# Kernel tuning notes

Measured on AMD Instinct MI355X. Metric: run time of the kernel, lower is better.

Reference implementation:

```python
import jax, jax.numpy as jnp
import numpy as np

D, HEADS, LVLS, PTS, DFF = 256, 8, 4, 4, 1024
LQ, B = 900, 16
SHAPES = [(100, 100), (50, 50), (25, 25), (13, 13)]
S = sum(h * w for h, w in SHAPES)  # 13294
EPS = 1e-5


def layer_norm(x, g, b):
    m = jnp.mean(x, -1, keepdims=True)
    v = jnp.mean((x - m) ** 2, -1, keepdims=True)
    return (x - m) * jax.lax.rsqrt(v + EPS) * g + b


def bilinear_gather(value_l, loc, H_, W_):
    # value_l: (b,h,H_,W_,dh); loc: (b,h,Lq,P,2) normalized to [0,1]
    b, h, _, _, dh = value_l.shape
    Lq, P = loc.shape[2], loc.shape[3]
    # grid_sample align_corners=False, padding_mode='zeros' semantics
    x = loc[..., 0] * W_ - 0.5
    y = loc[..., 1] * H_ - 0.5
    x0 = jnp.floor(x); y0 = jnp.floor(y)
    wx = x - x0; wy = y - y0
    x0i = x0.astype(jnp.int32); y0i = y0.astype(jnp.int32)
    vflat = value_l.reshape(b, h, H_ * W_, dh)

    def corner(xi, yi, w):
        valid = (xi >= 0) & (xi < W_) & (yi >= 0) & (yi < H_)
        idx = jnp.clip(yi, 0, H_ - 1) * W_ + jnp.clip(xi, 0, W_ - 1)
        g = jnp.take_along_axis(vflat, idx.reshape(b, h, Lq * P)[..., None], axis=2)
        return g.reshape(b, h, Lq, P, dh) * (w * valid)[..., None]

    return (corner(x0i, y0i, (1 - wx) * (1 - wy)) + corner(x0i + 1, y0i, wx * (1 - wy))
            + corner(x0i, y0i + 1, (1 - wx) * wy) + corner(x0i + 1, y0i + 1, wx * wy))


def setup_inputs() -> dict:
    key = jax.random.key(0)
    ks = jax.random.split(key, 32)
    w = lambda k, *s: (jax.random.normal(k, s, jnp.float32) * 0.02)
    shapes = jnp.array(SHAPES, jnp.int32)
    starts = jnp.array(np.cumsum([0] + [h_ * w_ for h_, w_ in SHAPES[:-1]]), jnp.int32)
    return {
        'tgt': jax.random.normal(ks[0], (LQ, B, D), jnp.float32),
        'tgt_query_pos': jax.random.normal(ks[1], (LQ, B, D), jnp.float32),
        'tgt_reference_points': jax.random.uniform(ks[2], (LQ, B, LVLS, 4), jnp.float32, 0.05, 0.95),
        'memory': jax.random.normal(ks[3], (S, B, D), jnp.float32),
        'memory_spatial_shapes': shapes,
        'memory_level_start_index': starts,
        # self-attn (nn.MultiheadAttention)
        'in_proj_w': w(ks[4], 3 * D, D), 'in_proj_b': jnp.zeros((3 * D,), jnp.float32),
        'sa_out_w': w(ks[5], D, D), 'sa_out_b': jnp.zeros((D,), jnp.float32),
        # MSDeformAttn
        'off_w': w(ks[6], HEADS * LVLS * PTS * 2, D), 'off_b': w(ks[7], HEADS * LVLS * PTS * 2),
        'aw_w': w(ks[8], HEADS * LVLS * PTS, D), 'aw_b': jnp.zeros((HEADS * LVLS * PTS,), jnp.float32),
        'val_w': w(ks[9], D, D), 'val_b': jnp.zeros((D,), jnp.float32),
        'ca_out_w': w(ks[10], D, D), 'ca_out_b': jnp.zeros((D,), jnp.float32),
        # FFN
        'lin1_w': w(ks[11], DFF, D), 'lin1_b': jnp.zeros((DFF,), jnp.float32),
        'lin2_w': w(ks[12], D, DFF), 'lin2_b': jnp.zeros((D,), jnp.float32),
        # norms (norm2 after sa, norm1 after ca, norm3 after ffn)
        'norm1_g': jnp.ones((D,), jnp.float32), 'norm1_b': jnp.zeros((D,), jnp.float32),
        'norm2_g': jnp.ones((D,), jnp.float32), 'norm2_b': jnp.zeros((D,), jnp.float32),
        'norm3_g': jnp.ones((D,), jnp.float32), 'norm3_b': jnp.zeros((D,), jnp.float32),
    }


def reference(tgt, tgt_query_pos, tgt_reference_points, memory,
              memory_spatial_shapes, memory_level_start_index,
              in_proj_w, in_proj_b, sa_out_w, sa_out_b,
              off_w, off_b, aw_w, aw_b, val_w, val_b, ca_out_w, ca_out_b,
              lin1_w, lin1_b, lin2_w, lin2_b,
              norm1_g, norm1_b, norm2_g, norm2_b, norm3_g, norm3_b):
    Lq, b, d = tgt.shape
    h = HEADS
    dh = d // h
    shapes = np.asarray(memory_spatial_shapes)  # static level shapes
    starts = np.asarray(memory_level_start_index)

    # ---- self-attention (module_seq[0] = 'sa') ----
    qk = tgt + tgt_query_pos  # pos on q,k only
    Wq, Wk, Wv = jnp.split(in_proj_w, 3, axis=0)
    bq, bk, bv = jnp.split(in_proj_b, 3)
    to_heads = lambda x: x.transpose(1, 0, 2).reshape(b, Lq, h, dh).transpose(0, 2, 1, 3)
    qh = to_heads(qk @ Wq.T + bq)
    kh = to_heads(qk @ Wk.T + bk)
    vh = to_heads(tgt @ Wv.T + bv)
    attn = jax.nn.softmax(jnp.einsum('bhqd,bhkd->bhqk', qh, kh) / jnp.sqrt(jnp.float32(dh)), axis=-1)
    sa = jnp.einsum('bhqk,bhkd->bhqd', attn, vh).transpose(0, 2, 1, 3).reshape(b, Lq, d).transpose(1, 0, 2)
    sa = sa @ sa_out_w.T + sa_out_b
    tgt = layer_norm(tgt + sa, norm2_g, norm2_b)

    # ---- deformable cross-attention (MSDeformAttn) ----
    query = (tgt + tgt_query_pos).transpose(1, 0, 2)            # (b,Lq,d)
    ref = tgt_reference_points.transpose(1, 0, 2, 3)            # (b,Lq,L,4)
    value = (memory.transpose(1, 0, 2) @ val_w.T + val_b).reshape(b, -1, h, dh)  # (b,S,h,dh)
    off = (query @ off_w.T + off_b).reshape(b, Lq, h, LVLS, PTS, 2)
    aw = jax.nn.softmax((query @ aw_w.T + aw_b).reshape(b, Lq, h, LVLS * PTS), axis=-1)
    aw = aw.reshape(b, Lq, h, LVLS, PTS).transpose(0, 2, 1, 3, 4)  # (b,h,Lq,L,P)
    # 4-dim refs: loc = xy + off/P * wh * 0.5
    loc = ref[:, :, None, :, None, :2] + off / PTS * ref[:, :, None, :, None, 2:] * 0.5
    loc = loc.transpose(0, 2, 1, 3, 4, 5)                        # (b,h,Lq,L,P,2)

    out = jnp.zeros((b, h, Lq, dh), jnp.float32)
    for l in range(LVLS):
        H_, W_ = int(shapes[l, 0]), int(shapes[l, 1])
        s0 = int(starts[l])
        value_l = value[:, s0:s0 + H_ * W_].reshape(b, H_, W_, h, dh).transpose(0, 3, 1, 2, 4)
        samp = bilinear_gather(value_l, loc[:, :, :, l], H_, W_)   # (b,h,Lq,P,dh)
        out = out + jnp.einsum('bhqpd,bhqp->bhqd', samp, aw[:, :, :, l])
    ca = out.transpose(0, 2, 1, 3).reshape(b, Lq, d) @ ca_out_w.T + ca_out_b
    ca = ca.transpose(1, 0, 2)
    tgt = layer_norm(tgt + ca, norm1_g, norm1_b)

    # ---- FFN (intended math: linear2(relu(linear1(tgt)))) ----
    t2 = jnp.maximum(tgt @ lin1_w.T + lin1_b, 0.0) @ lin2_w.T + lin2_b
    tgt = layer_norm(tgt + t2, norm3_g, norm3_b)
    return tgt
```

## Files before the change

kernel.cpp:

```cpp
#include <hip/hip_runtime.h>
#include <hip/hip_bf16.h>
#include <math.h>

#define D_ 256
#define HEADS_ 8
#define DH_ 32
#define LVLS_ 4
#define PTS_ 4
#define DFF_ 1024
#define LQ_ 900
#define B_ 16
#define S_ 13294
#define MQ (LQ_*B_)
#define MV (S_*B_)

typedef __attribute__((ext_vector_type(4))) float f32x4;
typedef __attribute__((ext_vector_type(8))) short bf16x8;

static __device__ inline ushort f2bf(float f) {
  __hip_bfloat16 h = __float2bfloat16(f);
  union { __hip_bfloat16 h; ushort u; } c; c.h = h;
  return c.u;
}
static __device__ inline float bf2f(ushort u) {
  union { float f; uint u; } c; c.u = (uint)u << 16; return c.f;
}

#define GP 40

__global__ __launch_bounds__(512) void gemm_bf16_512(
    const float* __restrict__ A, const float* __restrict__ Wm,
    const float* __restrict__ bias, float* __restrict__ Y,
    int M, int N, int K, int relu, int outbf)
{
  __shared__ ushort As[128 * GP];
  __shared__ ushort Ws[128 * GP];
  const int tid  = threadIdx.x;
  const int lane = tid & 63;
  const int wid  = tid >> 6;
  const int wr   = wid >> 1;
  const int wc   = wid & 1;
  const int fr = lane & 15;
  const int fk = (lane >> 4) << 3;
  const int m0 = blockIdx.y * 128, n0 = blockIdx.x * 128;

  f32x4 acc[2][4];
  const f32x4 zero = {0.f, 0.f, 0.f, 0.f};
#pragma unroll
  for (int i = 0; i < 2; ++i)
#pragma unroll
    for (int j = 0; j < 4; ++j) acc[i][j] = zero;

  const int srow = tid >> 2;
  const int skh  = (tid & 3) << 3;
  int agr = m0 + srow; if (agr > M - 1) agr = M - 1;
  const float* apb = A  + (size_t)agr * K + skh;
  const float* wpb = Wm + (size_t)(n0 + srow) * K + skh;

  float4 pa[2], pw[2];
  pa[0] = *(const float4*)(apb);     pa[1] = *(const float4*)(apb + 4);
  pw[0] = *(const float4*)(wpb);     pw[1] = *(const float4*)(wpb + 4);

  for (int k0 = 0; k0 < K; k0 += 32) {
    if (k0) __syncthreads();
    ushort tmp[8] __attribute__((aligned(16)));
    tmp[0]=f2bf(pa[0].x); tmp[1]=f2bf(pa[0].y); tmp[2]=f2bf(pa[0].z); tmp[3]=f2bf(pa[0].w);
    tmp[4]=f2bf(pa[1].x); tmp[5]=f2bf(pa[1].y); tmp[6]=f2bf(pa[1].z); tmp[7]=f2bf(pa[1].w);
    *(bf16x8*)&As[srow*GP + skh] = *(const bf16x8*)tmp;
    tmp[0]=f2bf(pw[0].x); tmp[1]=f2bf(pw[0].y); tmp[2]=f2bf(pw[0].z); tmp[3]=f2bf(pw[0].w);
    tmp[4]=f2bf(pw[1].x); tmp[5]=f2bf(pw[1].y); tmp[6]=f2bf(pw[1].z); tmp[7]=f2bf(pw[1].w);
    *(bf16x8*)&Ws[srow*GP + skh] = *(const bf16x8*)tmp;
    if (k0 + 32 < K) {
      const float* ap = apb + k0 + 32;
      const float* wp = wpb + k0 + 32;
      pa[0] = *(const float4*)(ap);  pa[1] = *(const float4*)(ap + 4);
      pw[0] = *(const float4*)(wp);  pw[1] = *(const float4*)(wp + 4);
    }
    __syncthreads();

    bf16x8 ar[2], br[4];
#pragma unroll
    for (int i = 0; i < 2; ++i)
      ar[i] = *(const bf16x8*)&As[(wr*32 + i*16 + fr)*GP + fk];
#pragma unroll
    for (int j = 0; j < 4; ++j)
      br[j] = *(const bf16x8*)&Ws[(wc*64 + j*16 + fr)*GP + fk];
#pragma unroll
    for (int i = 0; i < 2; ++i)
#pragma unroll
      for (int j = 0; j < 4; ++j)
        acc[i][j] = __builtin_amdgcn_mfma_f32_16x16x32_bf16(ar[i], br[j], acc[i][j], 0, 0, 0);
  }

  const int gcolbase = n0 + wc * 64 + fr;
  float bias4[4];
#pragma unroll
  for (int j = 0; j < 4; ++j) bias4[j] = bias[gcolbase + j * 16];
#pragma unroll
  for (int i = 0; i < 2; ++i) {
    const int rb = m0 + wr * 32 + i * 16 + (lane >> 4) * 4;
#pragma unroll
    for (int r = 0; r < 4; ++r) {
      const int grow = rb + r;
      if (grow < M) {
#pragma unroll
        for (int j = 0; j < 4; ++j) {
          float v = acc[i][j][r] + bias4[j];
          if (relu) v = fmaxf(v, 0.f);
          if (outbf) ((ushort*)Y)[(size_t)grow * N + gcolbase + j * 16] = f2bf(v);
          else       Y[(size_t)grow * N + gcolbase + j * 16] = v;
        }
      }
    }
  }
}

__global__ __launch_bounds__(256) void gemm_bf16_64(
    const float* __restrict__ A, const float* __restrict__ X2,
    const float* __restrict__ Wm, const float* __restrict__ bias,
    float* __restrict__ Y, int M, int N, int K, int relu, int outbf)
{
  __shared__ ushort As[64 * GP];
  __shared__ ushort Ws[64 * GP];
  const int tid  = threadIdx.x;
  const int lane = tid & 63;
  const int wid  = tid >> 6;
  const int wr = wid >> 1, wc = wid & 1;
  const int fr = lane & 15;
  const int fk = (lane >> 4) << 3;
  const int m0 = blockIdx.y * 64, n0 = blockIdx.x * 64;

  f32x4 acc[2][2];
  const f32x4 zero = {0.f, 0.f, 0.f, 0.f};
#pragma unroll
  for (int i = 0; i < 2; ++i)
#pragma unroll
    for (int j = 0; j < 2; ++j) acc[i][j] = zero;

  const int srow = tid >> 1;
  const int skh  = (tid & 1) << 4;
  const bool isA = srow < 64;
  const float* src;
  const float* src2 = nullptr;
  ushort* dst;
  if (isA) {
    int gr = m0 + srow; if (gr > M - 1) gr = M - 1;
    src = A + (size_t)gr * K + skh;
    if (X2) src2 = X2 + (size_t)gr * K + skh;
    dst = &As[srow * GP + skh];
  } else {
    src = Wm + (size_t)(n0 + srow - 64) * K + skh;
    dst = &Ws[(srow - 64) * GP + skh];
  }

  float4 pd[4];
#pragma unroll
  for (int i2 = 0; i2 < 4; ++i2) pd[i2] = *(const float4*)(src + i2 * 4);
  if (src2) {
#pragma unroll
    for (int i2 = 0; i2 < 4; ++i2) {
      const float4 u = *(const float4*)(src2 + i2 * 4);
      pd[i2].x += u.x; pd[i2].y += u.y; pd[i2].z += u.z; pd[i2].w += u.w;
    }
  }

  for (int k0 = 0; k0 < K; k0 += 32) {
    if (k0) __syncthreads();
    ushort tmp[16] __attribute__((aligned(16)));
#pragma unroll
    for (int i2 = 0; i2 < 4; ++i2) {
      tmp[i2*4+0] = f2bf(pd[i2].x); tmp[i2*4+1] = f2bf(pd[i2].y);
      tmp[i2*4+2] = f2bf(pd[i2].z); tmp[i2*4+3] = f2bf(pd[i2].w);
    }
    *(bf16x8*)(dst)     = *(const bf16x8*)&tmp[0];
    *(bf16x8*)(dst + 8) = *(const bf16x8*)&tmp[8];
    if (k0 + 32 < K) {
      const float* s = src + k0 + 32;
#pragma unroll
      for (int i2 = 0; i2 < 4; ++i2) pd[i2] = *(const float4*)(s + i2 * 4);
      if (src2) {
        const float* s2 = src2 + k0 + 32;
#pragma unroll
        for (int i2 = 0; i2 < 4; ++i2) {
          const float4 u = *(const float4*)(s2 + i2 * 4);
          pd[i2].x += u.x; pd[i2].y += u.y; pd[i2].z += u.z; pd[i2].w += u.w;
        }
      }
    }
    __syncthreads();

    bf16x8 af[2], bf[2];
#pragma unroll
    for (int i = 0; i < 2; ++i)
      af[i] = *(const bf16x8*)&As[(wr*32 + i*16 + fr)*GP + fk];
#pragma unroll
    for (int j = 0; j < 2; ++j)
      bf[j] = *(const bf16x8*)&Ws[(wc*32 + j*16 + fr)*GP + fk];
#pragma unroll
    for (int i = 0; i < 2; ++i)
#pragma unroll
      for (int j = 0; j < 2; ++j)
        acc[i][j] = __builtin_amdgcn_mfma_f32_16x16x32_bf16(af[i], bf[j], acc[i][j], 0, 0, 0);
  }

  const int gcolbase = n0 + wc * 32 + fr;
  float bias2[2];
#pragma unroll
  for (int j = 0; j < 2; ++j) bias2[j] = bias[gcolbase + j * 16];
#pragma unroll
  for (int i = 0; i < 2; ++i) {
    const int rb = m0 + wr * 32 + i * 16 + (lane >> 4) * 4;
#pragma unroll
    for (int r = 0; r < 4; ++r) {
      const int grow = rb + r;
      if (grow < M) {
#pragma unroll
        for (int j = 0; j < 2; ++j) {
          float v = acc[i][j][r] + bias2[j];
          if (relu) v = fmaxf(v, 0.f);
          if (outbf) ((ushort*)Y)[(size_t)grow * N + gcolbase + j * 16] = f2bf(v);
          else       Y[(size_t)grow * N + gcolbase + j * 16] = v;
        }
      }
    }
  }
}

__global__ __launch_bounds__(256) void gemm_bias_kernel(
    const float* __restrict__ X1, const float* __restrict__ X2,
    const float* __restrict__ W, const float* __restrict__ bias,
    float* __restrict__ Y, int M, int N, int K, int relu)
{
  __shared__ float As[16][64];
  __shared__ float Ws[16][64];
  const int tid = threadIdx.x;
  const int tx = tid & 15, ty = tid >> 4;
  const int m0 = blockIdx.y * 64, n0 = blockIdx.x * 64;
  float acc[4][4] = {};
  for (int k0 = 0; k0 < K; k0 += 16) {
    const int i   = tid * 4;
    const int row = i >> 4;
    const int col = i & 15;
    const int gr  = m0 + row;
    float4 v = make_float4(0.f, 0.f, 0.f, 0.f);
    if (gr < M) {
      v = *(const float4*)(X1 + (size_t)gr * K + k0 + col);
      if (X2) {
        float4 u = *(const float4*)(X2 + (size_t)gr * K + k0 + col);
        v.x += u.x; v.y += u.y; v.z += u.z; v.w += u.w;
      }
    }
    As[col+0][row] = v.x; As[col+1][row] = v.y; As[col+2][row] = v.z; As[col+3][row] = v.w;
    const float4 wv = *(const float4*)(W + (size_t)(n0 + row) * K + k0 + col);
    Ws[col+0][row] = wv.x; Ws[col+1][row] = wv.y; Ws[col+2][row] = wv.z; Ws[col+3][row] = wv.w;
    __syncthreads();
#pragma unroll
    for (int kk = 0; kk < 16; ++kk) {
      const float4 a = *(const float4*)&As[kk][ty * 4];
      const float4 w = *(const float4*)&Ws[kk][tx * 4];
      const float av[4] = {a.x, a.y, a.z, a.w};
      const float wv2[4] = {w.x, w.y, w.z, w.w};
#pragma unroll
      for (int ii = 0; ii < 4; ++ii)
#pragma unroll
        for (int jj = 0; jj < 4; ++jj)
          acc[ii][jj] = fmaf(av[ii], wv2[jj], acc[ii][jj]);
    }
    __syncthreads();
  }
  const float4 b4 = *(const float4*)(bias + n0 + tx * 4);
  const float bb[4] = {b4.x, b4.y, b4.z, b4.w};
#pragma unroll
  for (int ii = 0; ii < 4; ++ii) {
    const int gr = m0 + ty * 4 + ii;
    if (gr < M) {
      float4 o;
      o.x = acc[ii][0] + bb[0];
      o.y = acc[ii][1] + bb[1];
      o.z = acc[ii][2] + bb[2];
      o.w = acc[ii][3] + bb[3];
      if (relu) {
        o.x = fmaxf(o.x, 0.f); o.y = fmaxf(o.y, 0.f);
        o.z = fmaxf(o.z, 0.f); o.w = fmaxf(o.w, 0.f);
      }
      *(float4*)(Y + (size_t)gr * N + n0 + tx * 4) = o;
    }
  }
}

#define QB 64
#define KB 64
#define KP 40
#define VP 72
__global__ __launch_bounds__(256) void attn_mfma_kernel(
    const float* __restrict__ QK, const float* __restrict__ V,
    float* __restrict__ O)
{
  __shared__ ushort Ks[KB * KP];
  __shared__ ushort Vt[DH_ * VP];
  __shared__ ushort Pl[4][16 * KP];
  const int tid  = threadIdx.x;
  const int lane = tid & 63;
  const int w    = tid >> 6;
  const int bh = blockIdx.y;
  const int h  = bh & (HEADS_ - 1);
  const int b  = bh >> 3;
  const int q0 = blockIdx.x * QB;
  const int lq = lane & 15;
  const int lg = lane >> 4;
  const float scale = 0.17677669529663687f;
  const f32x4 zero4 = {0.f, 0.f, 0.f, 0.f};

  bf16x8 qf;
  {
    int qg = q0 + w * 16 + lq; if (qg > LQ_ - 1) qg = LQ_ - 1;
    const float* qp = QK + ((size_t)qg * B_ + b) * 512 + h * DH_ + lg * 8;
    const float4 a = *(const float4*)qp;
    const float4 c = *(const float4*)(qp + 4);
    ushort t[8] __attribute__((aligned(16)));
    t[0]=f2bf(a.x*scale); t[1]=f2bf(a.y*scale); t[2]=f2bf(a.z*scale); t[3]=f2bf(a.w*scale);
    t[4]=f2bf(c.x*scale); t[5]=f2bf(c.y*scale); t[6]=f2bf(c.z*scale); t[7]=f2bf(c.w*scale);
    qf = *(const bf16x8*)t;
  }

  float mrow = -1e30f, srow = 0.f;
  f32x4 oacc[2]; oacc[0] = zero4; oacc[1] = zero4;

  const int nkt = (LQ_ + KB - 1) / KB;
  for (int t = 0; t < nkt; ++t) {
    const int k0 = t * KB;
    const int klen = (LQ_ - k0) < KB ? (LQ_ - k0) : KB;
    if (t) __syncthreads();
    {
      const int kk  = tid >> 2;
      const int dh0 = (tid & 3) * 8;
      ushort kb[8] __attribute__((aligned(16)));
      ushort vb[8];
      if (kk < klen) {
        const size_t row = (size_t)(k0 + kk) * B_ + b;
        const float* kp = QK + row * 512 + 256 + h * DH_ + dh0;
        const float* vp = V  + row * 256 + h * DH_ + dh0;
        const float4 k1 = *(const float4*)kp;
        const float4 k2 = *(const float4*)(kp + 4);
        const float4 v1 = *(const float4*)vp;
        const float4 v2 = *(const float4*)(vp + 4);
        kb[0]=f2bf(k1.x); kb[1]=f2bf(k1.y); kb[2]=f2bf(k1.z); kb[3]=f2bf(k1.w);
        kb[4]=f2bf(k2.x); kb[5]=f2bf(k2.y); kb[6]=f2bf(k2.z); kb[7]=f2bf(k2.w);
        vb[0]=f2bf(v1.x); vb[1]=f2bf(v1.y); vb[2]=f2bf(v1.z); vb[3]=f2bf(v1.w);
        vb[4]=f2bf(v2.x); vb[5]=f2bf(v2.y); vb[6]=f2bf(v2.z); vb[7]=f2bf(v2.w);
      } else {
#pragma unroll
        for (int j = 0; j < 8; ++j) { kb[j] = 0; vb[j] = 0; }
      }
      *(bf16x8*)&Ks[kk * KP + dh0] = *(const bf16x8*)kb;
#pragma unroll
      for (int j = 0; j < 8; ++j) Vt[(dh0 + j) * VP + kk] = vb[j];
    }
    __syncthreads();

    f32x4 sc[4];
#pragma unroll
    for (int j = 0; j < 4; ++j) {
      const bf16x8 kf = *(const bf16x8*)&Ks[(j * 16 + lq) * KP + lg * 8];
      sc[j] = __builtin_amdgcn_mfma_f32_16x16x32_bf16(kf, qf, zero4, 0, 0, 0);
    }
    if (klen < KB) {
#pragma unroll
      for (int j = 0; j < 4; ++j)
#pragma unroll
        for (int r = 0; r < 4; ++r)
          if (j * 16 + lg * 4 + r >= klen) sc[j][r] = -1e30f;
    }
    float tmax = -1e30f;
#pragma unroll
    for (int j = 0; j < 4; ++j)
#pragma unroll
      for (int r = 0; r < 4; ++r) tmax = fmaxf(tmax, sc[j][r]);
    tmax = fmaxf(tmax, __shfl_xor(tmax, 16, 64));
    tmax = fmaxf(tmax, __shfl_xor(tmax, 32, 64));
    const float mnew = fmaxf(mrow, tmax);
    const float cfac = __expf(mrow - mnew);
    mrow = mnew;
    float tsum = 0.f;
#pragma unroll
    for (int j = 0; j < 4; ++j)
#pragma unroll
      for (int r = 0; r < 4; ++r) {
        const float p = __expf(sc[j][r] - mnew);
        sc[j][r] = p; tsum += p;
      }
    tsum += __shfl_xor(tsum, 16, 64);
    tsum += __shfl_xor(tsum, 32, 64);
    srow = srow * cfac + tsum;
#pragma unroll
    for (int j = 0; j < 4; ++j) {
      const uint lo = (uint)f2bf(sc[j][0]) | ((uint)f2bf(sc[j][1]) << 16);
      const uint hi = (uint)f2bf(sc[j][2]) | ((uint)f2bf(sc[j][3]) << 16);
      *(uint*)&Pl[w][lq * KP + j * 16 + lg * 4]     = lo;
      *(uint*)&Pl[w][lq * KP + j * 16 + lg * 4 + 2] = hi;
    }
    float crow[4];
#pragma unroll
    for (int r = 0; r < 4; ++r) crow[r] = __shfl(cfac, lg * 4 + r, 64);
#pragma unroll
    for (int nt = 0; nt < 2; ++nt)
#pragma unroll
      for (int r = 0; r < 4; ++r) oacc[nt][r] *= crow[r];
#pragma unroll
    for (int ks = 0; ks < 2; ++ks) {
      const bf16x8 pf = *(const bf16x8*)&Pl[w][lq * KP + ks * 32 + lg * 8];
#pragma unroll
      for (int nt = 0; nt < 2; ++nt) {
        const bf16x8 vf = *(const bf16x8*)&Vt[(nt * 16 + lq) * VP + ks * 32 + lg * 8];
        oacc[nt] = __builtin_amdgcn_mfma_f32_16x16x32_bf16(pf, vf, oacc[nt], 0, 0, 0);
      }
    }
  }
  float sinv[4];
#pragma unroll
  for (int r = 0; r < 4; ++r) {
    const float sr = __shfl(srow, lg * 4 + r, 64);
    sinv[r] = 1.f / sr;
  }
#pragma unroll
  for (int r = 0; r < 4; ++r) {
    const int qg = q0 + w * 16 + lg * 4 + r;
    if (qg < LQ_) {
      float* op = O + ((size_t)qg * B_ + b) * 256 + h * DH_;
      op[lq]      = oacc[0][r] * sinv[r];
      op[16 + lq] = oacc[1][r] * sinv[r];
    }
  }
}

__global__ __launch_bounds__(256) void ln_kernel(
    const float* __restrict__ X, const float* __restrict__ R,
    const float* __restrict__ g, const float* __restrict__ be,
    float* __restrict__ Y)
{
  const int row = blockIdx.x;
  const int t = threadIdx.x;
  const size_t idx = (size_t)row * D_ + t;
  const float v = X[idx] + R[idx];
  __shared__ float red[4];
  const int wid = t >> 6, lane = t & 63;

  float sum = v;
#pragma unroll
  for (int o = 32; o > 0; o >>= 1) sum += __shfl_xor(sum, o, 64);
  if (lane == 0) red[wid] = sum;
  __syncthreads();
  const float mean = (red[0] + red[1] + red[2] + red[3]) * (1.f / D_);
  const float d = v - mean;
  float sq = d * d;
#pragma unroll
  for (int o = 32; o > 0; o >>= 1) sq += __shfl_xor(sq, o, 64);
  __syncthreads();
  if (lane == 0) red[wid] = sq;
  __syncthreads();
  const float var = (red[0] + red[1] + red[2] + red[3]) * (1.f / D_);
  Y[idx] = d * rsqrtf(var + 1e-5f) * g[t] + be[t];
}

__global__ __launch_bounds__(256) void msdeform_kernel(
    const float* __restrict__ refp, const float* __restrict__ offb,
    const float* __restrict__ awb, const ushort* __restrict__ value,
    float* __restrict__ out)
{
  const int t  = blockIdx.x * 256 + threadIdx.x;
  const int dq = t & 3;
  const int h  = (t >> 2) & 7;
  const int u  = t >> 5;
  const int b  = u / LQ_;
  const int q  = u - b * LQ_;
  const int r  = q * B_ + b;

  float aw[LVLS_ * PTS_];
  const float* ap = awb + (size_t)r * 128 + h * 16;
  float m = -1e30f;
#pragma unroll
  for (int i = 0; i < 16; ++i) { aw[i] = ap[i]; m = fmaxf(m, aw[i]); }
  float s = 0.f;
#pragma unroll
  for (int i = 0; i < 16; ++i) { aw[i] = __expf(aw[i] - m); s += aw[i]; }
  const float inv = 1.f / s;
#pragma unroll
  for (int i = 0; i < 16; ++i) aw[i] *= inv;

  float o[8] = {};
  const int HH[4] = {100, 50, 25, 13};
  const int WW[4] = {100, 50, 25, 13};
  const int ST[4] = {0, 10000, 12500, 13125};
  const float* orow = offb + (size_t)r * 256 + h * (LVLS_ * PTS_ * 2);
  const int dh0 = h * DH_ + dq * 8;

  for (int l = 0; l < LVLS_; ++l) {
    const float4 rf = *(const float4*)(refp + (((size_t)q * B_ + b) * LVLS_ + l) * 4);
    const int W_ = WW[l], H_ = HH[l], s0 = ST[l];
    for (int p = 0; p < PTS_; ++p) {
      const float ox = orow[(l * PTS_ + p) * 2 + 0];
      const float oy = orow[(l * PTS_ + p) * 2 + 1];
      const float lx = rf.x + ox * 0.125f * rf.z;
      const float ly = rf.y + oy * 0.125f * rf.w;
      const float x = lx * W_ - 0.5f;
      const float y = ly * H_ - 0.5f;
      const float x0f = floorf(x), y0f = floorf(y);
      const float wx = x - x0f, wy = y - y0f;
      const int x0 = (int)x0f, y0 = (int)y0f;
      const float a = aw[l * PTS_ + p];
      const float cw[4] = {(1.f - wx) * (1.f - wy) * a, wx * (1.f - wy) * a,
                           (1.f - wx) * wy * a,         wx * wy * a};
      const int cx[4] = {x0, x0 + 1, x0, x0 + 1};
      const int cy[4] = {y0, y0, y0 + 1, y0 + 1};
#pragma unroll
      for (int c = 0; c < 4; ++c) {
        const int xi = cx[c], yi = cy[c];
        if (xi >= 0 && xi < W_ && yi >= 0 && yi < H_) {
          const ushort* vp = value + ((size_t)(s0 + yi * W_ + xi) * B_ + b) * 256 + dh0;
          const float w = cw[c];
          const bf16x8 vv = *(const bf16x8*)vp;
#pragma unroll
          for (int j = 0; j < 8; ++j)
            o[j] = fmaf(w, bf2f(((const ushort*)&vv)[j]), o[j]);
        }
      }
    }
  }
  float* op = out + (size_t)r * 256 + dh0;
  float4 x1; x1.x = o[0]; x1.y = o[1]; x1.z = o[2]; x1.w = o[3];
  float4 x2; x2.x = o[4]; x2.y = o[5]; x2.z = o[6]; x2.w = o[7];
  *(float4*)op = x1;
  *(float4*)(op + 4) = x2;
}

extern "C" void kernel_launch(void* const* d_in, const int* in_sizes, int n_in,
                              void* d_out, int out_size, void* d_ws, size_t ws_size,
                              hipStream_t stream) {
  const float* tgt       = (const float*)d_in[0];
  const float* pos       = (const float*)d_in[1];
  const float* refp      = (const float*)d_in[2];
  const float* memory    = (const float*)d_in[3];
  const float* in_proj_w = (const float*)d_in[6];
  const float* in_proj_b = (const float*)d_in[7];
  const float* sa_out_w  = (const float*)d_in[8];
  const float* sa_out_b  = (const float*)d_in[9];
  const float* off_w     = (const float*)d_in[10];
  const float* off_b     = (const float*)d_in[11];
  const float* aw_w      = (const float*)d_in[12];
  const float* aw_b      = (const float*)d_in[13];
  const float* val_w     = (const float*)d_in[14];
  const float* val_b     = (const float*)d_in[15];
  const float* ca_out_w  = (const float*)d_in[16];
  const float* ca_out_b  = (const float*)d_in[17];
  const float* lin1_w    = (const float*)d_in[18];
  const float* lin1_b    = (const float*)d_in[19];
  const float* lin2_w    = (const float*)d_in[20];
  const float* lin2_b    = (const float*)d_in[21];
  const float* n1g = (const float*)d_in[22];
  const float* n1b = (const float*)d_in[23];
  const float* n2g = (const float*)d_in[24];
  const float* n2b = (const float*)d_in[25];
  const float* n3g = (const float*)d_in[26];
  const float* n3b = (const float*)d_in[27];

  float* ws = (float*)d_ws;
  float* QK    = ws;
  float* Vb    = QK   + (size_t)MQ * 512;
  float* Cb    = Vb   + (size_t)MQ * 256;
  float* Db    = Cb   + (size_t)MQ * 256;
  float* tgt1  = Db   + (size_t)MQ * 256;
  float* tgt2  = tgt1 + (size_t)MQ * 256;
  float* big   = tgt2 + (size_t)MQ * 256;
  ushort* value = (ushort*)big;
  float* mid   = big;

  const dim3 blk(256);
  const int gy_q = (MQ + 63) / 64;
  const int gy_v128 = (MV + 127) / 128;
  const int qtiles = (LQ_ + QB - 1) / QB;

  gemm_bf16_64<<<dim3(8, gy_q), blk, 0, stream>>>(tgt, pos, in_proj_w, in_proj_b, QK, MQ, 512, D_, 0, 0);
  gemm_bf16_64<<<dim3(4, gy_q), blk, 0, stream>>>(tgt, nullptr, in_proj_w + 512 * D_, in_proj_b + 512, Vb, MQ, 256, D_, 0, 0);
  attn_mfma_kernel<<<dim3(qtiles, B_ * HEADS_), blk, 0, stream>>>(QK, Vb, Cb);
  gemm_bf16_64<<<dim3(4, gy_q), blk, 0, stream>>>(Cb, nullptr, sa_out_w, sa_out_b, Db, MQ, 256, D_, 0, 0);
  ln_kernel<<<MQ, blk, 0, stream>>>(tgt, Db, n2g, n2b, tgt1);
  gemm_bf16_512<<<dim3(2, gy_v128), dim3(512), 0, stream>>>(memory, val_w, val_b, (float*)value, MV, 256, D_, 0, 1);
  gemm_bias_kernel<<<dim3(4, gy_q), blk, 0, stream>>>(tgt1, pos, off_w, off_b, QK, MQ, 256, D_, 0);
  gemm_bf16_64<<<dim3(2, gy_q), blk, 0, stream>>>(tgt1, pos, aw_w, aw_b, Vb, MQ, 128, D_, 0, 0);
  msdeform_kernel<<<(MQ * HEADS_ * 4 + 255) / 256, blk, 0, stream>>>(refp, QK, Vb, value, Cb);
  gemm_bf16_64<<<dim3(4, gy_q), blk, 0, stream>>>(Cb, nullptr, ca_out_w, ca_out_b, Db, MQ, 256, D_, 0, 0);
  ln_kernel<<<MQ, blk, 0, stream>>>(tgt1, Db, n1g, n1b, tgt2);
  gemm_bf16_64<<<dim3(16, gy_q), blk, 0, stream>>>(tgt2, nullptr, lin1_w, lin1_b, mid, MQ, DFF_, D_, 1, 0);
  gemm_bf16_64<<<dim3(4, gy_q), blk, 0, stream>>>(mid, nullptr, lin2_w, lin2_b, Db, MQ, 256, DFF_, 0, 0);
  ln_kernel<<<MQ, blk, 0, stream>>>(tgt2, Db, n3g, n3b, (float*)d_out);
}
```

Before: 557.0 us.

## Specialize value-projection GEMM: full weight tile in swizzled LDS, direct A loads

The value projection GEMM now loads the whole 128x256 weight slice into shared memory once, with an XOR swizzle against bank conflicts. The A operand is read straight from global memory into registers in MFMA fragment layout and converted to bf16, with no LDS staging. This removes the per-k-step __syncthreads and the shared-memory round trip for A, and hardcodes K=256 and bf16 output. In exchange it uses 64KB of LDS per block, which limits occupancy, and the global A loads are less coalesced.

```diff
diff --git a/kernel.cpp b/kernel.cpp
--- a/kernel.cpp
+++ b/kernel.cpp
@@ -28,21 +28,33 @@
 
 #define GP 40
 
-__global__ __launch_bounds__(512) void gemm_bf16_512(
+__global__ __launch_bounds__(512) void gemm_val_kernel(
     const float* __restrict__ A, const float* __restrict__ Wm,
-    const float* __restrict__ bias, float* __restrict__ Y,
-    int M, int N, int K, int relu, int outbf)
+    const float* __restrict__ bias, ushort* __restrict__ Y, int M)
 {
-  __shared__ ushort As[128 * GP];
-  __shared__ ushort Ws[128 * GP];
+  __shared__ ushort Ws[128 * 256];
   const int tid  = threadIdx.x;
   const int lane = tid & 63;
   const int wid  = tid >> 6;
   const int wr   = wid >> 1;
   const int wc   = wid & 1;
   const int fr = lane & 15;
-  const int fk = (lane >> 4) << 3;
+  const int hi = lane >> 4;
+  const int fk = hi << 3;
   const int m0 = blockIdx.y * 128, n0 = blockIdx.x * 128;
+
+#pragma unroll
+  for (int c = 0; c < 16; ++c) {
+    const int f    = c * 512 + tid;
+    const int row  = f >> 6;
+    const int col4 = f & 63;
+    const float4 v = *(const float4*)(Wm + (((size_t)(n0 + row)) << 8) + col4 * 4);
+    ushort t4[4] __attribute__((aligned(8)));
+    t4[0] = f2bf(v.x); t4[1] = f2bf(v.y); t4[2] = f2bf(v.z); t4[3] = f2bf(v.w);
+    const int ui = row * 256 + ((col4 * 4) ^ ((row & 7) << 3));
+    *(uint2*)&Ws[ui] = *(const uint2*)t4;
+  }
+  __syncthreads();
 
   f32x4 acc[2][4];
   const f32x4 zero = {0.f, 0.f, 0.f, 0.f};
@@ -51,40 +63,33 @@
 #pragma unroll
     for (int j = 0; j < 4; ++j) acc[i][j] = zero;
 
-  const int srow = tid >> 2;
-  const int skh  = (tid & 3) << 3;
-  int agr = m0 + srow; if (agr > M - 1) agr = M - 1;
-  const float* apb = A  + (size_t)agr * K + skh;
-  const float* wpb = Wm + (size_t)(n0 + srow) * K + skh;
-
-  float4 pa[2], pw[2];
-  pa[0] = *(const float4*)(apb);     pa[1] = *(const float4*)(apb + 4);
-  pw[0] = *(const float4*)(wpb);     pw[1] = *(const float4*)(wpb + 4);
-
-  for (int k0 = 0; k0 < K; k0 += 32) {
-    if (k0) __syncthreads();
-    ushort tmp[8] __attribute__((aligned(16)));
-    tmp[0]=f2bf(pa[0].x); tmp[1]=f2bf(pa[0].y); tmp[2]=f2bf(pa[0].z); tmp[3]=f2bf(pa[0].w);
-    tmp[4]=f2bf(pa[1].x); tmp[5]=f2bf(pa[1].y); tmp[6]=f2bf(pa[1].z); tmp[7]=f2bf(pa[1].w);
-    *(bf16x8*)&As[srow*GP + skh] = *(const bf16x8*)tmp;
-    tmp[0]=f2bf(pw[0].x); tmp[1]=f2bf(pw[0].y); tmp[2]=f2bf(pw[0].z); tmp[3]=f2bf(pw[0].w);
-    tmp[4]=f2bf(pw[1].x); tmp[5]=f2bf(pw[1].y); tmp[6]=f2bf(pw[1].z); tmp[7]=f2bf(pw[1].w);
-    *(bf16x8*)&Ws[srow*GP + skh] = *(const bf16x8*)tmp;
-    if (k0 + 32 < K) {
-      const float* ap = apb + k0 + 32;
-      const float* wp = wpb + k0 + 32;
-      pa[0] = *(const float4*)(ap);  pa[1] = *(const float4*)(ap + 4);
-      pw[0] = *(const float4*)(wp);  pw[1] = *(const float4*)(wp + 4);
-    }
-    __syncthreads();
-
+  uint aoff[2];
+#pragma unroll
+  for (int i = 0; i < 2; ++i) {
+    int r = m0 + wr * 32 + i * 16 + fr;
+    if (r > M - 1) r = M - 1;
+    aoff[i] = (uint)r * 256u + (uint)fk;
+  }
+  const int rsw = (fr & 7) << 3;
+
+#pragma unroll
+  for (int k0 = 0; k0 < 256; k0 += 32) {
     bf16x8 ar[2], br[4];
 #pragma unroll
-    for (int i = 0; i < 2; ++i)
-      ar[i] = *(const bf16x8*)&As[(wr*32 + i*16 + fr)*GP + fk];
-#pragma unroll
-    for (int j = 0; j < 4; ++j)
-      br[j] = *(const bf16x8*)&Ws[(wc*64 + j*16 + fr)*GP + fk];
+    for (int i = 0; i < 2; ++i) {
+      const float* p = A + aoff[i] + k0;
+      const float4 lo = *(const float4*)p;
+      const float4 h4 = *(const float4*)(p + 4);
+      ushort t[8] __attribute__((aligned(16)));
+      t[0]=f2bf(lo.x); t[1]=f2bf(lo.y); t[2]=f2bf(lo.z); t[3]=f2bf(lo.w);
+      t[4]=f2bf(h4.x); t[5]=f2bf(h4.y); t[6]=f2bf(h4.z); t[7]=f2bf(h4.w);
+      ar[i] = *(const bf16x8*)t;
+    }
+#pragma unroll
+    for (int j = 0; j < 4; ++j) {
+      const int nrow = wc * 64 + j * 16 + fr;
+      br[j] = *(const bf16x8*)&Ws[nrow * 256 + ((k0 + fk) ^ rsw)];
+    }
 #pragma unroll
     for (int i = 0; i < 2; ++i)
 #pragma unroll
@@ -98,18 +103,14 @@
   for (int j = 0; j < 4; ++j) bias4[j] = bias[gcolbase + j * 16];
 #pragma unroll
   for (int i = 0; i < 2; ++i) {
-    const int rb = m0 + wr * 32 + i * 16 + (lane >> 4) * 4;
+    const int rb = m0 + wr * 32 + i * 16 + hi * 4;
 #pragma unroll
     for (int r = 0; r < 4; ++r) {
       const int grow = rb + r;
       if (grow < M) {
 #pragma unroll
-        for (int j = 0; j < 4; ++j) {
-          float v = acc[i][j][r] + bias4[j];
-          if (relu) v = fmaxf(v, 0.f);
-          if (outbf) ((ushort*)Y)[(size_t)grow * N + gcolbase + j * 16] = f2bf(v);
-          else       Y[(size_t)grow * N + gcolbase + j * 16] = v;
-        }
+        for (int j = 0; j < 4; ++j)
+          Y[(size_t)grow * 256 + gcolbase + j * 16] = f2bf(acc[i][j][r] + bias4[j]);
       }
     }
   }
@@ -584,7 +585,7 @@
   attn_mfma_kernel<<<dim3(qtiles, B_ * HEADS_), blk, 0, stream>>>(QK, Vb, Cb);
   gemm_bf16_64<<<dim3(4, gy_q), blk, 0, stream>>>(Cb, nullptr, sa_out_w, sa_out_b, Db, MQ, 256, D_, 0, 0);
   ln_kernel<<<MQ, blk, 0, stream>>>(tgt, Db, n2g, n2b, tgt1);
-  gemm_bf16_512<<<dim3(2, gy_v128), dim3(512), 0, stream>>>(memory, val_w, val_b, (float*)value, MV, 256, D_, 0, 1);
+  gemm_val_kernel<<<dim3(2, gy_v128), dim3(512), 0, stream>>>(memory, val_w, val_b, value, MV);
   gemm_bias_kernel<<<dim3(4, gy_q), blk, 0, stream>>>(tgt1, pos, off_w, off_b, QK, MQ, 256, D_, 0);
   gemm_bf16_64<<<dim3(2, gy_q), blk, 0, stream>>>(tgt1, pos, aw_w, aw_b, Vb, MQ, 128, D_, 0, 0);
   msdeform_kernel<<<(MQ * HEADS_ * 4 + 255) / 256, blk, 0, stream>>>(refp, QK, Vb, value, Cb);
```

New measurement: 583.8 us. 4.8% more time.
